# Kernel tuning notes

Measured on AMD Instinct MI355X. Metric: run time of the kernel, lower is better.

## Reference

```python
import jax, jax.numpy as jnp
import numpy as np

N_NODES = 100000
N_EDGES = 1600000
IN_CH = 128
HID = 128
OUT_CH = 16
N_GRAPHS = 64


def setup_inputs() -> dict:
    key = jax.random.key(0)
    ks = jax.random.split(key, 8)
    x = jax.random.normal(ks[0], (N_NODES, IN_CH), dtype=jnp.float32)
    edge_index = jax.random.randint(ks[1], (2, N_EDGES), 0, N_NODES, dtype=jnp.int64)
    batch = jnp.sort(jax.random.randint(ks[2], (N_NODES,), 0, N_GRAPHS, dtype=jnp.int64))
    s1 = 1.0 / np.sqrt(IN_CH)
    s2 = 1.0 / np.sqrt(HID)
    W1 = jax.random.uniform(ks[3], (IN_CH, HID), jnp.float32, -s1, s1)
    b1 = jnp.zeros((HID,), jnp.float32)
    W2 = jax.random.uniform(ks[4], (HID, HID), jnp.float32, -s2, s2)
    b2 = jnp.zeros((HID,), jnp.float32)
    Wfc = jax.random.uniform(ks[5], (HID, OUT_CH), jnp.float32, -s2, s2)
    bfc = jax.random.uniform(ks[6], (OUT_CH,), jnp.float32, -s2, s2)
    return {"x": x, "W1": W1, "b1": b1, "W2": W2, "b2": b2,
            "Wfc": Wfc, "bfc": bfc, "edge_index": edge_index, "batch": batch}


def _gcn_conv(x, W, b, src, dst, deg_inv_sqrt, deg_inv):
    # GCNConv with self-loops: out = D^-1/2 (A+I) D^-1/2 (x W) + b
    h = x @ W                                   # [N, H]
    norm = deg_inv_sqrt[src] * deg_inv_sqrt[dst]  # [E]
    agg = jax.ops.segment_sum(h[src] * norm[:, None], dst, num_segments=N_NODES)
    # self-loop term: deg_inv_sqrt[i]^2 * h[i]
    return agg + h * deg_inv[:, None] + b


def reference(x, W1, b1, W2, b2, Wfc, bfc, edge_index, batch):
    src, dst = edge_index[0], edge_index[1]
    # degree including self-loop
    deg = jax.ops.segment_sum(jnp.ones((N_EDGES,), jnp.float32), dst, num_segments=N_NODES) + 1.0
    deg_inv_sqrt = jax.lax.rsqrt(deg)
    deg_inv = 1.0 / deg
    h = jax.nn.relu(_gcn_conv(x, W1, b1, src, dst, deg_inv_sqrt, deg_inv))
    h = jax.nn.relu(_gcn_conv(h, W2, b2, src, dst, deg_inv_sqrt, deg_inv))
    # global mean pool over graphs
    sums = jax.ops.segment_sum(h, batch, num_segments=N_GRAPHS)          # [G, H]
    counts = jax.ops.segment_sum(jnp.ones((N_NODES,), jnp.float32), batch, num_segments=N_GRAPHS)
    pooled = sums / jnp.maximum(counts, 1.0)[:, None]
    return pooled @ Wfc + bfc
```

## Files before the change

### kernel.cpp

```cpp
#include <hip/hip_runtime.h>
#include <math.h>

#define NN 100000
#define NE 1600000
#define CH 128
#define OUTC 16
#define NG 64

#define CBSH 9
#define NCB 196
#define CHK 8192
#define MAXB 12288
#define PS 8
#define LDA 136

typedef __attribute__((ext_vector_type(8))) short bf16x8;
typedef __attribute__((ext_vector_type(4))) float f32x4;

__device__ __forceinline__ unsigned short f2bf(float f) {
    union { float f; unsigned u; } v; v.f = f;
    unsigned r = v.u + 0x7FFF + ((v.u >> 16) & 1);
    return (unsigned short)(r >> 16);
}
__device__ __forceinline__ float bflo(unsigned u) {
    union { unsigned u; float f; } v; v.u = u << 16; return v.f;
}
__device__ __forceinline__ float bfhi(unsigned u) {
    union { unsigned u; float f; } v; v.u = u & 0xffff0000u; return v.f;
}

__global__ void k_prep(const float* __restrict__ W1, const float* __restrict__ W2,
                       unsigned short* __restrict__ wt1, unsigned short* __restrict__ wt2,
                       const int* __restrict__ batch, int* __restrict__ gptr,
                       int* __restrict__ bcnt, int* __restrict__ gfill,
                       float* __restrict__ pooled, int* __restrict__ done) {
    int i = blockIdx.x * 256 + threadIdx.x;
    if (i < CH * CH) {
        int k = i >> 7, n = i & 127;
        wt1[n * CH + k] = f2bf(W1[i]);
    } else if (i < 2 * CH * CH) {
        int j = i - CH * CH;
        int k = j >> 7, n = j & 127;
        wt2[n * CH + k] = f2bf(W2[j]);
    }
    if (i < NCB) { bcnt[i] = 0; gfill[i] = 0; }
    if (i < NG * CH) pooled[i] = 0.f;
    if (i == 0) *done = 0;
    if (i < NN) {
        int b = batch[i];
        int prev = (i == 0) ? -1 : batch[i - 1];
        for (int g = prev + 1; g <= b; g++) gptr[g] = i;
        if (i == NN - 1) {
            for (int g = b + 1; g <= NG; g++) gptr[g] = NN;
        }
    }
}

__global__ __launch_bounds__(1024) void k_hist(const int* __restrict__ dst, int* __restrict__ bcnt) {
    __shared__ int h[NCB];
    int t = threadIdx.x;
    if (t < NCB) h[t] = 0;
    __syncthreads();
    int base = blockIdx.x * CHK;
#pragma unroll
    for (int i = 0; i < 8; i++) {
        int e = base + i * 1024 + t;
        if (e < NE) atomicAdd(&h[dst[e] >> CBSH], 1);
    }
    __syncthreads();
    if (t < NCB && h[t]) atomicAdd(&bcnt[t], h[t]);
}

__global__ __launch_bounds__(1024) void k_passA(const int* __restrict__ src, const int* __restrict__ dst,
                        const int* __restrict__ bcnt, int* __restrict__ gfill,
                        unsigned* __restrict__ ebuf) {
    __shared__ unsigned lbuf[CHK];
    __shared__ unsigned char lbyte[CHK];
    __shared__ int hcnt[NCB];
    __shared__ int hbase[256];
    __shared__ int eb[256];
    __shared__ int goff[NCB];
    int t = threadIdx.x;
    if (t < NCB) hcnt[t] = 0;
    if (t < 256) eb[t] = (t < NCB) ? bcnt[t] : 0;
    __syncthreads();
    int base = blockIdx.x * CHK;
    int cb[8], slot[8]; unsigned pk[8];
#pragma unroll
    for (int i = 0; i < 8; i++) {
        int e = base + i * 1024 + t;
        cb[i] = -1;
        if (e < NE) {
            int d = dst[e], s = src[e];
            cb[i] = d >> CBSH;
            pk[i] = ((unsigned)s << CBSH) | (unsigned)(d & 511);
            slot[i] = atomicAdd(&hcnt[cb[i]], 1);
        }
    }
    __syncthreads();
    if (t < 256) hbase[t] = (t < NCB) ? hcnt[t] : 0;
    __syncthreads();
    for (int off = 1; off < 256; off <<= 1) {
        int v1 = 0, v2 = 0;
        if (t < 256 && t >= off) { v1 = hbase[t - off]; v2 = eb[t - off]; }
        __syncthreads();
        if (t < 256 && t >= off) { hbase[t] += v1; eb[t] += v2; }
        __syncthreads();
    }
    if (t < NCB) {
        int c = hcnt[t];
        int g = c ? atomicAdd(&gfill[t], c) : 0;
        int ebase_t = t ? eb[t - 1] : 0;
        goff[t] = ebase_t + g - (hbase[t] - c);
    }
    __syncthreads();
#pragma unroll
    for (int i = 0; i < 8; i++) {
        if (cb[i] >= 0) {
            int pos = hbase[cb[i]] - hcnt[cb[i]] + slot[i];
            lbuf[pos] = pk[i];
            lbyte[pos] = (unsigned char)cb[i];
        }
    }
    __syncthreads();
    int total = min(NE - base, CHK);
    for (int p = t; p < total; p += 1024) {
        unsigned v = lbuf[p];
        int b = lbyte[p];
        ebuf[goff[b] + p] = v;
    }
}

__global__ __launch_bounds__(1024) void k_passB(const unsigned* __restrict__ ebuf, const int* __restrict__ bcnt,
                        int* __restrict__ degi, int* __restrict__ rowst,
                        float* __restrict__ dis, int* __restrict__ csr) {
    __shared__ int cnt[512];
    __shared__ int nbase[512];
    __shared__ int fill[512];
    __shared__ int stage[MAXB];
    __shared__ int eb[256];
    int t = threadIdx.x;
    int cb = blockIdx.x;
    int nb0 = cb << CBSH;
    int ncnt = min(512, NN - nb0);
    if (t < 512) { cnt[t] = 0; fill[t] = 0; }
    if (t < 256) eb[t] = (t < NCB) ? bcnt[t] : 0;
    __syncthreads();
    for (int off = 1; off < 256; off <<= 1) {
        int v = 0;
        if (t < 256 && t >= off) v = eb[t - off];
        __syncthreads();
        if (t < 256 && t >= off) eb[t] += v;
        __syncthreads();
    }
    int e0 = cb ? eb[cb - 1] : 0;
    int e1 = eb[cb];
    for (int e = e0 + t; e < e1; e += 1024)
        atomicAdd(&cnt[ebuf[e] & 511], 1);
    __syncthreads();
    if (t < 512) nbase[t] = cnt[t];
    __syncthreads();
    for (int off = 1; off < 512; off <<= 1) {
        int v = 0;
        if (t < 512 && t >= off) v = nbase[t - off];
        __syncthreads();
        if (t < 512) nbase[t] += v;
        __syncthreads();
    }
    for (int e = e0 + t; e < e1; e += 1024) {
        unsigned v = ebuf[e];
        int local = v & 511;
        int s = atomicAdd(&fill[local], 1);
        stage[nbase[local] - cnt[local] + s] = (int)(v >> CBSH);
    }
    __syncthreads();
    int total = e1 - e0;
    for (int p = t; p < total; p += 1024) csr[e0 + p] = stage[p];
    if (t < ncnt) {
        int c = cnt[t];
        degi[nb0 + t] = c;
        rowst[nb0 + t] = e0 + nbase[t] - c;
        dis[nb0 + t] = rsqrtf((float)c + 1.0f);
    }
}

template<bool F32IN>
__launch_bounds__(256, 2)
__global__ void k_gemm(const void* __restrict__ Av,
                       const unsigned short* __restrict__ WT,
                       const float* __restrict__ dis,
                       unsigned short* __restrict__ out) {
    __shared__ unsigned short As[128 * LDA];
    int tid = threadIdx.x;
    int wave = tid >> 6, lane = tid & 63;
    int quad = lane >> 4, l16 = lane & 15;

    int rbase = blockIdx.x * 128;
    int nval = min(128, NN - rbase);

    if (F32IN) {
        const float* X = (const float*)Av + (size_t)rbase * CH;
#pragma unroll
        for (int i = 0; i < 16; i++) {
            int off = i * 1024 + tid * 4;
            int row = off >> 7, col = off & 127;
            if (row < nval) {
                float4 f = *(const float4*)(X + (size_t)row * CH + col);
                uint2 pk;
                pk.x = (unsigned)f2bf(f.x) | ((unsigned)f2bf(f.y) << 16);
                pk.y = (unsigned)f2bf(f.z) | ((unsigned)f2bf(f.w) << 16);
                *(uint2*)(&As[row * LDA + col]) = pk;
            }
        }
    } else {
        const unsigned short* X = (const unsigned short*)Av + (size_t)rbase * CH;
#pragma unroll
        for (int i = 0; i < 8; i++) {
            int off = i * 2048 + tid * 8;
            int row = off >> 7, col = off & 127;
            if (row < nval) {
                bf16x8 v = *(const bf16x8*)(X + (size_t)row * CH + col);
                *(bf16x8*)(&As[row * LDA + col]) = v;
            }
        }
    }
    __syncthreads();

    int wrow = wave * 32;
    bf16x8 af[2][4];
#pragma unroll
    for (int s = 0; s < 2; s++)
#pragma unroll
        for (int ks = 0; ks < 4; ks++)
            af[s][ks] = *(const bf16x8*)(&As[(wrow + s * 16 + l16) * LDA + ks * 32 + quad * 8]);

    f32x4 acc[2][8];
#pragma unroll
    for (int s = 0; s < 2; s++)
#pragma unroll
        for (int t = 0; t < 8; t++) acc[s][t] = (f32x4){0.f, 0.f, 0.f, 0.f};

#pragma unroll
    for (int t = 0; t < 8; t++) {
        const unsigned short* wcol = WT + (size_t)(t * 16 + l16) * CH + quad * 8;
        bf16x8 b0 = *(const bf16x8*)(wcol);
        bf16x8 b1 = *(const bf16x8*)(wcol + 32);
        bf16x8 b2 = *(const bf16x8*)(wcol + 64);
        bf16x8 b3 = *(const bf16x8*)(wcol + 96);
#pragma unroll
        for (int s = 0; s < 2; s++) {
            acc[s][t] = __builtin_amdgcn_mfma_f32_16x16x32_bf16(b0, af[s][0], acc[s][t], 0, 0, 0);
            acc[s][t] = __builtin_amdgcn_mfma_f32_16x16x32_bf16(b1, af[s][1], acc[s][t], 0, 0, 0);
            acc[s][t] = __builtin_amdgcn_mfma_f32_16x16x32_bf16(b2, af[s][2], acc[s][t], 0, 0, 0);
            acc[s][t] = __builtin_amdgcn_mfma_f32_16x16x32_bf16(b3, af[s][3], acc[s][t], 0, 0, 0);
        }
    }

#pragma unroll
    for (int s = 0; s < 2; s++) {
        int node = rbase + wrow + s * 16 + l16;
        int cl = (node < NN) ? node : NN - 1;
        float d = dis[cl];
        if (node < NN) {
#pragma unroll
            for (int t = 0; t < 8; t++) {
                unsigned lo = ((unsigned)f2bf(acc[s][t][1] * d) << 16) | (unsigned)f2bf(acc[s][t][0] * d);
                unsigned hi = ((unsigned)f2bf(acc[s][t][3] * d) << 16) | (unsigned)f2bf(acc[s][t][2] * d);
                uint2 pk; pk.x = lo; pk.y = hi;
                *(uint2*)(out + (size_t)node * CH + t * 16 + quad * 4) = pk;
            }
        }
    }
}

__global__ __launch_bounds__(256) void k_agg(const unsigned short* __restrict__ ht, const int* __restrict__ rowst,
                      const int* __restrict__ degi, const int* __restrict__ csr,
                      const float* __restrict__ dis, const float* __restrict__ bias,
                      unsigned short* __restrict__ out) {
    int t = threadIdx.x;
    int grp = t >> 4;
    int q = t & 15;
    int n = blockIdx.x * 16 + grp;
    const uint4* base = (const uint4*)ht;

    uint4 sv = base[(size_t)n * 16 + q];
    float a[8];
    a[0] = bflo(sv.x); a[1] = bfhi(sv.x);
    a[2] = bflo(sv.y); a[3] = bfhi(sv.y);
    a[4] = bflo(sv.z); a[5] = bfhi(sv.z);
    a[6] = bflo(sv.w); a[7] = bfhi(sv.w);

    int start = rowst[n];
    int c = degi[n];
    int nb = c & ~7;
    int j = 0;
    for (; j < nb; j += 8) {
        int idx[8];
#pragma unroll
        for (int u = 0; u < 8; u++) idx[u] = csr[start + j + u];
        uint4 v[8];
#pragma unroll
        for (int u = 0; u < 8; u++) v[u] = base[(size_t)idx[u] * 16 + q];
#pragma unroll
        for (int u = 0; u < 8; u++) {
            a[0] += bflo(v[u].x); a[1] += bfhi(v[u].x);
            a[2] += bflo(v[u].y); a[3] += bfhi(v[u].y);
            a[4] += bflo(v[u].z); a[5] += bfhi(v[u].z);
            a[6] += bflo(v[u].w); a[7] += bfhi(v[u].w);
        }
    }
    if (j < c) {
        int idx[8];
#pragma unroll
        for (int u = 0; u < 8; u++) { int e = j + u; idx[u] = csr[start + (e < c ? e : c - 1)]; }
        uint4 v[8];
#pragma unroll
        for (int u = 0; u < 8; u++) v[u] = base[(size_t)idx[u] * 16 + q];
#pragma unroll
        for (int u = 0; u < 8; u++) {
            if (j + u < c) {
                a[0] += bflo(v[u].x); a[1] += bfhi(v[u].x);
                a[2] += bflo(v[u].y); a[3] += bfhi(v[u].y);
                a[4] += bflo(v[u].z); a[5] += bfhi(v[u].z);
                a[6] += bflo(v[u].w); a[7] += bfhi(v[u].w);
            }
        }
    }

    float d = dis[n];
    const float4* bp = (const float4*)bias;
    float4 b0 = bp[q * 2], b1 = bp[q * 2 + 1];
    uint4 o;
    {
        float ox = fmaxf(fmaf(d, a[0], b0.x), 0.f), oy = fmaxf(fmaf(d, a[1], b0.y), 0.f);
        o.x = ((unsigned)f2bf(oy) << 16) | (unsigned)f2bf(ox);
        ox = fmaxf(fmaf(d, a[2], b0.z), 0.f); oy = fmaxf(fmaf(d, a[3], b0.w), 0.f);
        o.y = ((unsigned)f2bf(oy) << 16) | (unsigned)f2bf(ox);
        ox = fmaxf(fmaf(d, a[4], b1.x), 0.f); oy = fmaxf(fmaf(d, a[5], b1.y), 0.f);
        o.z = ((unsigned)f2bf(oy) << 16) | (unsigned)f2bf(ox);
        ox = fmaxf(fmaf(d, a[6], b1.z), 0.f); oy = fmaxf(fmaf(d, a[7], b1.w), 0.f);
        o.w = ((unsigned)f2bf(oy) << 16) | (unsigned)f2bf(ox);
    }
    ((uint4*)out)[(size_t)n * 16 + q] = o;
}

__global__ __launch_bounds__(512) void k_pool_final(const unsigned short* __restrict__ h,
                                               const int* __restrict__ gptr,
                                               float* __restrict__ pooled,
                                               int* __restrict__ done,
                                               const float* __restrict__ Wfc,
                                               const float* __restrict__ bfc,
                                               float* __restrict__ out) {
    int g = blockIdx.x >> 3;
    int s = blockIdx.x & 7;
    int gs = gptr[g], ge = gptr[g + 1];
    int len = ge - gs;
    int i0 = gs + (int)(((long long)len * s) >> 3);
    int i1 = gs + (int)(((long long)len * (s + 1)) >> 3);
    int t = threadIdx.x;
    int pr = t & 63;
    int ro = t >> 6;
    const unsigned* base = (const unsigned*)h;
    float s0 = 0.f, s1 = 0.f;
    for (int n = i0 + ro; n < i1; n += 8) {
        unsigned v = base[(size_t)n * 64 + pr];
        s0 += bflo(v); s1 += bfhi(v);
    }
    __shared__ float red[2][8][64];
    red[0][ro][pr] = s0; red[1][ro][pr] = s1;
    __syncthreads();
    for (int off = 4; off >= 1; off >>= 1) {
        if (ro < off) {
            red[0][ro][pr] += red[0][ro + off][pr];
            red[1][ro][pr] += red[1][ro + off][pr];
        }
        __syncthreads();
    }
    if (ro == 0) {
        atomicAdd(&pooled[g * CH + pr * 2],     red[0][0][pr]);
        atomicAdd(&pooled[g * CH + pr * 2 + 1], red[1][0][pr]);
    }

    __shared__ int lastFlag;
    __shared__ float plds[NG * CH];
    __syncthreads();
    if (t == 0) {
        __threadfence();
        int r = atomicAdd(done, 1);
        lastFlag = (r == NG * PS - 1) ? 1 : 0;
    }
    __syncthreads();
    if (!lastFlag) return;
    for (int i = t; i < NG * CH; i += 512) plds[i] = atomicAdd(&pooled[i], 0.0f);
    __syncthreads();
    for (int idx = t; idx < NG * OUTC; idx += 512) {
        int gg = idx >> 4, o = idx & 15;
        float c = (float)(gptr[gg + 1] - gptr[gg]);
        float inv = 1.0f / fmaxf(c, 1.0f);
        float acc = 0.f;
        for (int k = 0; k < CH; k++) acc += plds[gg * CH + k] * Wfc[k * OUTC + o];
        out[idx] = fmaf(acc, inv, bfc[o]);
    }
}

extern "C" void kernel_launch(void* const* d_in, const int* in_sizes, int n_in,
                              void* d_out, int out_size, void* d_ws, size_t ws_size,
                              hipStream_t stream) {
    (void)in_sizes; (void)n_in; (void)out_size; (void)ws_size;
    const float* x   = (const float*)d_in[0];
    const float* W1  = (const float*)d_in[1];
    const float* b1  = (const float*)d_in[2];
    const float* W2  = (const float*)d_in[3];
    const float* b2  = (const float*)d_in[4];
    const float* Wfc = (const float*)d_in[5];
    const float* bfc = (const float*)d_in[6];
    const int* ei    = (const int*)d_in[7];
    const int* batch = (const int*)d_in[8];
    const int* esrc = ei;
    const int* edst = ei + NE;
    float* out = (float*)d_out;

    char* w = (char*)d_ws;
    unsigned short* bufA = (unsigned short*)w; w += (size_t)NN * CH * 2;
    unsigned short* bufB = (unsigned short*)w; w += (size_t)NN * CH * 2;
    unsigned short* wt1  = (unsigned short*)w; w += (size_t)CH * CH * 2;
    unsigned short* wt2  = (unsigned short*)w; w += (size_t)CH * CH * 2;
    unsigned* ebuf = (unsigned*)w; w += (size_t)NE * 4;
    int* csr    = (int*)w;    w += (size_t)NE * 4;
    int* degi   = (int*)w;    w += (size_t)NN * 4;
    int* rowst  = (int*)w;    w += (size_t)NN * 4;
    float* dis  = (float*)w;  w += (size_t)NN * 4;
    int* bcnt   = (int*)w;    w += NCB * 4;
    int* gfill  = (int*)w;    w += NCB * 4;
    int* gptr   = (int*)w;    w += (NG + 1) * 4;
    float* pooled = (float*)w; w += (size_t)NG * CH * 4;
    int* done   = (int*)w;    w += 4;

    const int histBlocks = (NE + CHK - 1) / CHK;
    const int gemmBlocks = (NN + 127) / 128;
    const int aggBlocks  = NN / 16;

    k_prep<<<(NN + 255) / 256, 256, 0, stream>>>(W1, W2, wt1, wt2, batch, gptr, bcnt, gfill, pooled, done);
    k_hist<<<histBlocks, 1024, 0, stream>>>(edst, bcnt);
    k_passA<<<histBlocks, 1024, 0, stream>>>(esrc, edst, bcnt, gfill, ebuf);
    k_passB<<<NCB, 1024, 0, stream>>>(ebuf, bcnt, degi, rowst, dis, csr);

    k_gemm<true><<<gemmBlocks, 256, 0, stream>>>(x, wt1, dis, bufA);
    k_agg<<<aggBlocks, 256, 0, stream>>>(bufA, rowst, degi, csr, dis, b1, bufB);
    k_gemm<false><<<gemmBlocks, 256, 0, stream>>>(bufB, wt2, dis, bufA);
    k_agg<<<aggBlocks, 256, 0, stream>>>(bufA, rowst, degi, csr, dis, b2, bufB);

    k_pool_final<<<NG * PS, 512, 0, stream>>>(bufB, gptr, pooled, done, Wfc, bfc, out);
}
```

Before: 336.0 us.

## Fuse layer-2 GEMM into first aggregation and mean-pool into second

The first aggregation kernel now stages each block's 16 aggregated rows in shared memory and runs the 128x128 layer-2 projection with MFMA before writing, which removes the separate GEMM kernel and a full bf16 round trip of the hidden activations. The second aggregation kernel reduces its 16 rows per graph segment in shared memory and atomically accumulates into the pooled sums. The last block to finish computes the final FC, so the separate pooling kernel and the re-read of the hidden state are gone. The cost is far more global atomics on the pooled array (6250 blocks times 128 channels) and extra shared-memory pressure in the aggregation kernels.

```diff
diff --git a/kernel.cpp b/kernel.cpp
--- a/kernel.cpp
+++ b/kernel.cpp
@@ -11,8 +11,8 @@
 #define NCB 196
 #define CHK 8192
 #define MAXB 12288
-#define PS 8
 #define LDA 136
+#define AGB (NN / 16)
 
 typedef __attribute__((ext_vector_type(8))) short bf16x8;
 typedef __attribute__((ext_vector_type(4))) float f32x4;
@@ -184,12 +184,11 @@
     }
 }
 
-template<bool F32IN>
 __launch_bounds__(256, 2)
-__global__ void k_gemm(const void* __restrict__ Av,
-                       const unsigned short* __restrict__ WT,
-                       const float* __restrict__ dis,
-                       unsigned short* __restrict__ out) {
+__global__ void k_gemm1(const float* __restrict__ Av,
+                        const unsigned short* __restrict__ WT,
+                        const float* __restrict__ dis,
+                        unsigned short* __restrict__ out) {
     __shared__ unsigned short As[128 * LDA];
     int tid = threadIdx.x;
     int wave = tid >> 6, lane = tid & 63;
@@ -198,30 +197,17 @@
     int rbase = blockIdx.x * 128;
     int nval = min(128, NN - rbase);
 
-    if (F32IN) {
-        const float* X = (const float*)Av + (size_t)rbase * CH;
-#pragma unroll
-        for (int i = 0; i < 16; i++) {
-            int off = i * 1024 + tid * 4;
-            int row = off >> 7, col = off & 127;
-            if (row < nval) {
-                float4 f = *(const float4*)(X + (size_t)row * CH + col);
-                uint2 pk;
-                pk.x = (unsigned)f2bf(f.x) | ((unsigned)f2bf(f.y) << 16);
-                pk.y = (unsigned)f2bf(f.z) | ((unsigned)f2bf(f.w) << 16);
-                *(uint2*)(&As[row * LDA + col]) = pk;
-            }
-        }
-    } else {
-        const unsigned short* X = (const unsigned short*)Av + (size_t)rbase * CH;
-#pragma unroll
-        for (int i = 0; i < 8; i++) {
-            int off = i * 2048 + tid * 8;
-            int row = off >> 7, col = off & 127;
-            if (row < nval) {
-                bf16x8 v = *(const bf16x8*)(X + (size_t)row * CH + col);
-                *(bf16x8*)(&As[row * LDA + col]) = v;
-            }
+    const float* X = Av + (size_t)rbase * CH;
+#pragma unroll
+    for (int i = 0; i < 16; i++) {
+        int off = i * 1024 + tid * 4;
+        int row = off >> 7, col = off & 127;
+        if (row < nval) {
+            float4 f = *(const float4*)(X + (size_t)row * CH + col);
+            uint2 pk;
+            pk.x = (unsigned)f2bf(f.x) | ((unsigned)f2bf(f.y) << 16);
+            pk.y = (unsigned)f2bf(f.z) | ((unsigned)f2bf(f.w) << 16);
+            *(uint2*)(&As[row * LDA + col]) = pk;
         }
     }
     __syncthreads();
@@ -273,14 +259,18 @@
     }
 }
 
-__global__ __launch_bounds__(256) void k_agg(const unsigned short* __restrict__ ht, const int* __restrict__ rowst,
+__global__ __launch_bounds__(256) void k_agg_gemm(const unsigned short* __restrict__ ht,
+                      const int* __restrict__ rowst,
                       const int* __restrict__ degi, const int* __restrict__ csr,
                       const float* __restrict__ dis, const float* __restrict__ bias,
+                      const unsigned short* __restrict__ WT,
                       unsigned short* __restrict__ out) {
+    __shared__ unsigned short As[16 * LDA];
     int t = threadIdx.x;
     int grp = t >> 4;
     int q = t & 15;
-    int n = blockIdx.x * 16 + grp;
+    int n0 = blockIdx.x * 16;
+    int n = n0 + grp;
     const uint4* base = (const uint4*)ht;
 
     uint4 sv = base[(size_t)n * 16 + q];
@@ -341,64 +331,136 @@
         ox = fmaxf(fmaf(d, a[6], b1.z), 0.f); oy = fmaxf(fmaf(d, a[7], b1.w), 0.f);
         o.w = ((unsigned)f2bf(oy) << 16) | (unsigned)f2bf(ox);
     }
-    ((uint4*)out)[(size_t)n * 16 + q] = o;
-}
-
-__global__ __launch_bounds__(512) void k_pool_final(const unsigned short* __restrict__ h,
-                                               const int* __restrict__ gptr,
-                                               float* __restrict__ pooled,
-                                               int* __restrict__ done,
-                                               const float* __restrict__ Wfc,
-                                               const float* __restrict__ bfc,
-                                               float* __restrict__ out) {
-    int g = blockIdx.x >> 3;
-    int s = blockIdx.x & 7;
-    int gs = gptr[g], ge = gptr[g + 1];
-    int len = ge - gs;
-    int i0 = gs + (int)(((long long)len * s) >> 3);
-    int i1 = gs + (int)(((long long)len * (s + 1)) >> 3);
+    *(uint4*)(&As[grp * LDA + q * 8]) = o;
+    __syncthreads();
+
+    int wave = t >> 6, lane = t & 63;
+    int l16 = lane & 15, quad = lane >> 4;
+    bf16x8 af2[4];
+#pragma unroll
+    for (int ks = 0; ks < 4; ks++)
+        af2[ks] = *(const bf16x8*)(&As[l16 * LDA + ks * 32 + quad * 8]);
+    int node = n0 + l16;
+    float dd = dis[node];
+#pragma unroll
+    for (int tt = 0; tt < 2; tt++) {
+        int tc = wave * 2 + tt;
+        const unsigned short* wcol = WT + (size_t)(tc * 16 + l16) * CH + quad * 8;
+        f32x4 acc = (f32x4){0.f, 0.f, 0.f, 0.f};
+        acc = __builtin_amdgcn_mfma_f32_16x16x32_bf16(*(const bf16x8*)(wcol),      af2[0], acc, 0, 0, 0);
+        acc = __builtin_amdgcn_mfma_f32_16x16x32_bf16(*(const bf16x8*)(wcol + 32), af2[1], acc, 0, 0, 0);
+        acc = __builtin_amdgcn_mfma_f32_16x16x32_bf16(*(const bf16x8*)(wcol + 64), af2[2], acc, 0, 0, 0);
+        acc = __builtin_amdgcn_mfma_f32_16x16x32_bf16(*(const bf16x8*)(wcol + 96), af2[3], acc, 0, 0, 0);
+        unsigned lo = ((unsigned)f2bf(acc[1] * dd) << 16) | (unsigned)f2bf(acc[0] * dd);
+        unsigned hi = ((unsigned)f2bf(acc[3] * dd) << 16) | (unsigned)f2bf(acc[2] * dd);
+        uint2 pk; pk.x = lo; pk.y = hi;
+        *(uint2*)(out + (size_t)node * CH + tc * 16 + quad * 4) = pk;
+    }
+}
+
+__global__ __launch_bounds__(256) void k_agg_pool(const unsigned short* __restrict__ ht,
+                      const int* __restrict__ rowst,
+                      const int* __restrict__ degi, const int* __restrict__ csr,
+                      const float* __restrict__ dis, const float* __restrict__ bias,
+                      const int* __restrict__ batch, const int* __restrict__ gptr,
+                      float* __restrict__ pooled, int* __restrict__ done,
+                      const float* __restrict__ Wfc, const float* __restrict__ bfc,
+                      float* __restrict__ out) {
+    __shared__ float sm[NG * CH];
+    float (*part)[132] = (float (*)[132])sm;
     int t = threadIdx.x;
-    int pr = t & 63;
-    int ro = t >> 6;
-    const unsigned* base = (const unsigned*)h;
-    float s0 = 0.f, s1 = 0.f;
-    for (int n = i0 + ro; n < i1; n += 8) {
-        unsigned v = base[(size_t)n * 64 + pr];
-        s0 += bflo(v); s1 += bfhi(v);
-    }
-    __shared__ float red[2][8][64];
-    red[0][ro][pr] = s0; red[1][ro][pr] = s1;
-    __syncthreads();
-    for (int off = 4; off >= 1; off >>= 1) {
-        if (ro < off) {
-            red[0][ro][pr] += red[0][ro + off][pr];
-            red[1][ro][pr] += red[1][ro + off][pr];
-        }
-        __syncthreads();
-    }
-    if (ro == 0) {
-        atomicAdd(&pooled[g * CH + pr * 2],     red[0][0][pr]);
-        atomicAdd(&pooled[g * CH + pr * 2 + 1], red[1][0][pr]);
+    int grp = t >> 4;
+    int q = t & 15;
+    int n0 = blockIdx.x * 16;
+    int n = n0 + grp;
+    const uint4* base = (const uint4*)ht;
+
+    uint4 sv = base[(size_t)n * 16 + q];
+    float a[8];
+    a[0] = bflo(sv.x); a[1] = bfhi(sv.x);
+    a[2] = bflo(sv.y); a[3] = bfhi(sv.y);
+    a[4] = bflo(sv.z); a[5] = bfhi(sv.z);
+    a[6] = bflo(sv.w); a[7] = bfhi(sv.w);
+
+    int start = rowst[n];
+    int c = degi[n];
+    int nb = c & ~7;
+    int j = 0;
+    for (; j < nb; j += 8) {
+        int idx[8];
+#pragma unroll
+        for (int u = 0; u < 8; u++) idx[u] = csr[start + j + u];
+        uint4 v[8];
+#pragma unroll
+        for (int u = 0; u < 8; u++) v[u] = base[(size_t)idx[u] * 16 + q];
+#pragma unroll
+        for (int u = 0; u < 8; u++) {
+            a[0] += bflo(v[u].x); a[1] += bfhi(v[u].x);
+            a[2] += bflo(v[u].y); a[3] += bfhi(v[u].y);
+            a[4] += bflo(v[u].z); a[5] += bfhi(v[u].z);
+            a[6] += bflo(v[u].w); a[7] += bfhi(v[u].w);
+        }
+    }
+    if (j < c) {
+        int idx[8];
+#pragma unroll
+        for (int u = 0; u < 8; u++) { int e = j + u; idx[u] = csr[start + (e < c ? e : c - 1)]; }
+        uint4 v[8];
+#pragma unroll
+        for (int u = 0; u < 8; u++) v[u] = base[(size_t)idx[u] * 16 + q];
+#pragma unroll
+        for (int u = 0; u < 8; u++) {
+            if (j + u < c) {
+                a[0] += bflo(v[u].x); a[1] += bfhi(v[u].x);
+                a[2] += bflo(v[u].y); a[3] += bfhi(v[u].y);
+                a[4] += bflo(v[u].z); a[5] += bfhi(v[u].z);
+                a[6] += bflo(v[u].w); a[7] += bfhi(v[u].w);
+            }
+        }
+    }
+
+    float d = dis[n];
+    const float4* bp = (const float4*)bias;
+    float4 b0 = bp[q * 2], b1 = bp[q * 2 + 1];
+    float4 r0, r1;
+    r0.x = fmaxf(fmaf(d, a[0], b0.x), 0.f); r0.y = fmaxf(fmaf(d, a[1], b0.y), 0.f);
+    r0.z = fmaxf(fmaf(d, a[2], b0.z), 0.f); r0.w = fmaxf(fmaf(d, a[3], b0.w), 0.f);
+    r1.x = fmaxf(fmaf(d, a[4], b1.x), 0.f); r1.y = fmaxf(fmaf(d, a[5], b1.y), 0.f);
+    r1.z = fmaxf(fmaf(d, a[6], b1.z), 0.f); r1.w = fmaxf(fmaf(d, a[7], b1.w), 0.f);
+    *(float4*)(&part[grp][q * 8])     = r0;
+    *(float4*)(&part[grp][q * 8 + 4]) = r1;
+    __syncthreads();
+
+    if (t < CH) {
+        int ch = t;
+        float s = 0.f;
+        int g = batch[n0];
+#pragma unroll
+        for (int gg = 0; gg < 16; gg++) {
+            int b = batch[n0 + gg];
+            if (b != g) { atomicAdd(&pooled[g * CH + ch], s); s = 0.f; g = b; }
+            s += part[gg][ch];
+        }
+        atomicAdd(&pooled[g * CH + ch], s);
     }
 
     __shared__ int lastFlag;
-    __shared__ float plds[NG * CH];
     __syncthreads();
     if (t == 0) {
         __threadfence();
         int r = atomicAdd(done, 1);
-        lastFlag = (r == NG * PS - 1) ? 1 : 0;
+        lastFlag = (r == AGB - 1) ? 1 : 0;
     }
     __syncthreads();
     if (!lastFlag) return;
-    for (int i = t; i < NG * CH; i += 512) plds[i] = atomicAdd(&pooled[i], 0.0f);
-    __syncthreads();
-    for (int idx = t; idx < NG * OUTC; idx += 512) {
+    for (int i = t; i < NG * CH; i += 256) sm[i] = atomicAdd(&pooled[i], 0.0f);
+    __syncthreads();
+    for (int idx = t; idx < NG * OUTC; idx += 256) {
         int gg = idx >> 4, o = idx & 15;
-        float c = (float)(gptr[gg + 1] - gptr[gg]);
-        float inv = 1.0f / fmaxf(c, 1.0f);
+        float cc = (float)(gptr[gg + 1] - gptr[gg]);
+        float inv = 1.0f / fmaxf(cc, 1.0f);
         float acc = 0.f;
-        for (int k = 0; k < CH; k++) acc += plds[gg * CH + k] * Wfc[k * OUTC + o];
+        for (int k = 0; k < CH; k++) acc += sm[gg * CH + k] * Wfc[k * OUTC + o];
         out[idx] = fmaf(acc, inv, bfc[o]);
     }
 }
@@ -438,17 +500,14 @@
 
     const int histBlocks = (NE + CHK - 1) / CHK;
     const int gemmBlocks = (NN + 127) / 128;
-    const int aggBlocks  = NN / 16;
 
     k_prep<<<(NN + 255) / 256, 256, 0, stream>>>(W1, W2, wt1, wt2, batch, gptr, bcnt, gfill, pooled, done);
     k_hist<<<histBlocks, 1024, 0, stream>>>(edst, bcnt);
     k_passA<<<histBlocks, 1024, 0, stream>>>(esrc, edst, bcnt, gfill, ebuf);
     k_passB<<<NCB, 1024, 0, stream>>>(ebuf, bcnt, degi, rowst, dis, csr);
 
-    k_gemm<true><<<gemmBlocks, 256, 0, stream>>>(x, wt1, dis, bufA);
-    k_agg<<<aggBlocks, 256, 0, stream>>>(bufA, rowst, degi, csr, dis, b1, bufB);
-    k_gemm<false><<<gemmBlocks, 256, 0, stream>>>(bufB, wt2, dis, bufA);
-    k_agg<<<aggBlocks, 256, 0, stream>>>(bufA, rowst, degi, csr, dis, b2, bufB);
-
-    k_pool_final<<<NG * PS, 512, 0, stream>>>(bufB, gptr, pooled, done, Wfc, bfc, out);
-}
+    k_gemm1<<<gemmBlocks, 256, 0, stream>>>(x, wt1, dis, bufA);
+    k_agg_gemm<<<AGB, 256, 0, stream>>>(bufA, rowst, degi, csr, dis, b1, wt2, bufB);
+    k_agg_pool<<<AGB, 256, 0, stream>>>(bufB, rowst, degi, csr, dis, b2, batch, gptr,
+                                        pooled, done, Wfc, bfc, out);
+}
```

Result: slower. 478.2 us (+42.3%).
